# Optimization experiments

Hardware: AMD Instinct MI355X
Metric: run time of the kernel (lower is better)

Reference implementation:

```python
import jax, jax.numpy as jnp
import numpy as np

B, L, HID, H, D = 1, 2048, 3072, 24, 128
MLP = 4 * HID
LH, LW = 32, 56      # latent mask grid -> LH*LW image tokens at the END of the sequence
LIP = 16             # IP-adapter image tokens
IP_SCALE = 0.6


def setup_inputs() -> dict:
    key = jax.random.key(0)
    k = jax.random.split(key, 10)
    # Flux rotary pe layout [1,1,L,D//2,2,2]: pe[...,0]=[cos,-sin], pe[...,1]=[sin,cos]
    pos = jnp.arange(L, dtype=jnp.float32)
    freqs = 1.0 / (10000.0 ** (jnp.arange(0, D, 2, dtype=jnp.float32) / D))
    ang = pos[:, None] * freqs[None, :]            # [L, D//2]
    cos, sin = jnp.cos(ang), jnp.sin(ang)
    pe = jnp.stack([jnp.stack([cos, -sin], -1), jnp.stack([sin, cos], -1)], -2)[None, None]
    return {
        "x": jax.random.normal(k[0], (B, L, HID), jnp.float32),
        "vec": jax.random.normal(k[1], (B, HID), jnp.float32),
        "pe": pe,
        "img_mask": jax.random.uniform(k[2], (B, LH, LW), jnp.float32),
        "image_emb": jax.random.normal(k[3], (B, LIP, HID), jnp.float32),
        "mod_w": jax.random.normal(k[4], (3 * HID, HID), jnp.float32) * 0.02,
        "mod_b": jnp.zeros((3 * HID,), jnp.float32),
        "lin1_w": jax.random.normal(k[5], (3 * HID + MLP, HID), jnp.float32) * 0.02,
        "lin1_b": jnp.zeros((3 * HID + MLP,), jnp.float32),
        "q_scale": jnp.ones((D,), jnp.float32),
        "k_scale": jnp.ones((D,), jnp.float32),
        "lin2_w": jax.random.normal(k[6], (HID, HID + MLP), jnp.float32) * 0.02,
        "lin2_b": jnp.zeros((HID,), jnp.float32),
        "ipk_w": jax.random.normal(k[7], (HID, HID), jnp.float32) * 0.02,
        "ipv_w": jax.random.normal(k[8], (HID, HID), jnp.float32) * 0.02,
    }


def _rms(x, scale, eps):
    # RMSNorm over last dim (QKNorm / norm_added_k)
    return x * jax.lax.rsqrt(jnp.mean(x * x, -1, keepdims=True) + eps) * scale


def _apply_rope(x, pe):
    # x: [B,H,L,D]; pe: [1,1,L,D//2,2,2]
    xr = x.reshape(x.shape[:-1] + (D // 2, 1, 2))
    out = pe[..., 0] * xr[..., 0] + pe[..., 1] * xr[..., 1]  # [B,H,L,D//2,2]
    return out.reshape(x.shape)


def _sdpa(q, k, v):
    # q:[B,H,Lq,D] k,v:[B,H,Lk,D] -> [B,Lq,H*D]
    s = jnp.einsum('bhqd,bhkd->bhqk', q, k) / jnp.sqrt(jnp.float32(D))
    o = jnp.einsum('bhqk,bhkd->bhqd', jax.nn.softmax(s, -1), v)
    return o.transpose(0, 2, 1, 3).reshape(q.shape[0], q.shape[2], H * D)


def reference(x, vec, pe, img_mask, image_emb, mod_w, mod_b, lin1_w, lin1_b,
              q_scale, k_scale, lin2_w, lin2_b, ipk_w, ipv_w):
    # modulation: SiLU(vec) -> Linear -> (shift, scale, gate), each [B,1,HID]
    mod = jax.nn.silu(vec) @ mod_w.T + mod_b
    shift, scale, gate = [m[:, None, :] for m in jnp.split(mod, 3, -1)]
    # pre_norm: LayerNorm, no affine, eps 1e-6 (biased variance, matches torch)
    ln = (x - jnp.mean(x, -1, keepdims=True)) * jax.lax.rsqrt(jnp.var(x, -1, keepdims=True) + 1e-6)
    x_mod = (1.0 + scale) * ln + shift
    # fused qkv + mlp projection
    h = x_mod @ lin1_w.T + lin1_b
    qkv, mlp = h[..., :3 * HID], h[..., 3 * HID:]
    q, k, v = qkv.reshape(B, L, 3, H, D).transpose(2, 0, 3, 1, 4)  # each [B,H,L,D]
    q = _rms(q, q_scale, 1e-6)
    k = _rms(k, k_scale, 1e-6)
    # rp_attention: RoPE then SDPA
    attn = _sdpa(_apply_rope(q, pe), _apply_rope(k, pe), v)       # [B,L,HID]
    # IP-adapter cross-attention: pre-rope q attends to projected image_emb
    ip_k = _rms((image_emb @ ipk_w.T).reshape(B, LIP, H, D).transpose(0, 2, 1, 3), 1.0, 1e-5)
    ip_v = (image_emb @ ipv_w.T).reshape(B, LIP, H, D).transpose(0, 2, 1, 3)
    ip_h = IP_SCALE * _sdpa(q, ip_k, ip_v)                        # [B,L,HID]
    # spatial mask applied to last LH*LW tokens, zeros elsewhere
    full_mask = jnp.concatenate(
        [jnp.zeros((B, L - LH * LW), ip_h.dtype), img_mask.reshape(B, LH * LW)], 1)
    attn = attn + ip_h * full_mask[..., None]
    out = jnp.concatenate([attn, jax.nn.gelu(mlp, approximate=True)], -1) @ lin2_w.T + lin2_b
    return x + gate * out
```

## Files before the change

kernel.cpp:

```cpp
#include <hip/hip_runtime.h>

#define HID 3072
#define LSEQ 2048
#define NH 24
#define HD 128
#define N1 21504
#define K2 15360

typedef unsigned short ushort_t;
typedef __attribute__((ext_vector_type(8))) short bf16x8;
typedef __attribute__((ext_vector_type(4))) float f32x4;

__device__ __forceinline__ unsigned short f2bf(float f) {
    union { float f; unsigned int u; } v; v.f = f;
    unsigned int u = v.u;
    u += 0x7fffu + ((u >> 16) & 1u);
    return (unsigned short)(u >> 16);
}
__device__ __forceinline__ float bf2f(unsigned short s) {
    union { unsigned int u; float f; } v; v.u = ((unsigned int)s) << 16;
    return v.f;
}
__device__ __forceinline__ float gelu_tanh(float x) {
    float u = 0.7978845608028654f * (x + 0.044715f * x * x * x);
    float t = 2.0f / (1.0f + __expf(-2.0f * u)) - 1.0f;
    return 0.5f * x * (1.0f + t);
}
__device__ __forceinline__ void gload_lds16(const ushort_t* g, ushort_t* l) {
    __builtin_amdgcn_global_load_lds((const __attribute__((address_space(1))) void*)g,
                                     (__attribute__((address_space(3))) void*)l, 16, 0, 0);
}

__global__ __launch_bounds__(256) void k_cvt2(const float* __restrict__ s1,
    ushort_t* __restrict__ d1, int n1, const float* __restrict__ s2,
    ushort_t* __restrict__ d2, int n2)
{
    int stride = gridDim.x * 256 * 8;
    int base = (blockIdx.x * 256 + threadIdx.x) * 8;
    for (int i = base; i < n1; i += stride) {
        float4 a = *reinterpret_cast<const float4*>(s1 + i);
        float4 b = *reinterpret_cast<const float4*>(s1 + i + 4);
        uint4 pk;
        pk.x = (unsigned)f2bf(a.x) | ((unsigned)f2bf(a.y) << 16);
        pk.y = (unsigned)f2bf(a.z) | ((unsigned)f2bf(a.w) << 16);
        pk.z = (unsigned)f2bf(b.x) | ((unsigned)f2bf(b.y) << 16);
        pk.w = (unsigned)f2bf(b.z) | ((unsigned)f2bf(b.w) << 16);
        *reinterpret_cast<uint4*>(d1 + i) = pk;
    }
    for (int i = base; i < n2; i += stride) {
        float4 a = *reinterpret_cast<const float4*>(s2 + i);
        float4 b = *reinterpret_cast<const float4*>(s2 + i + 4);
        uint4 pk;
        pk.x = (unsigned)f2bf(a.x) | ((unsigned)f2bf(a.y) << 16);
        pk.y = (unsigned)f2bf(a.z) | ((unsigned)f2bf(a.w) << 16);
        pk.z = (unsigned)f2bf(b.x) | ((unsigned)f2bf(b.y) << 16);
        pk.w = (unsigned)f2bf(b.z) | ((unsigned)f2bf(b.w) << 16);
        *reinterpret_cast<uint4*>(d2 + i) = pk;
    }
}

__global__ __launch_bounds__(256) void k_mod(const float* __restrict__ vec,
    const float* __restrict__ mw, const float* __restrict__ mb, float* __restrict__ mod) {
    __shared__ __align__(16) float sv[HID];
    int tid = threadIdx.x;
    for (int i = tid; i < HID; i += 256) {
        float v = vec[i];
        sv[i] = v / (1.0f + __expf(-v));
    }
    __syncthreads();
    int wave = tid >> 6, lane = tid & 63;
    int n = blockIdx.x * 4 + wave;
    const float* w = mw + (size_t)n * HID;
    float acc = 0.0f;
    for (int k = lane * 4; k < HID; k += 256) {
        float4 wv = *reinterpret_cast<const float4*>(w + k);
        float4 s  = *reinterpret_cast<const float4*>(sv + k);
        acc += wv.x * s.x + wv.y * s.y + wv.z * s.z + wv.w * s.w;
    }
    #pragma unroll
    for (int off = 1; off < 64; off <<= 1) acc += __shfl_xor(acc, off);
    if (lane == 0) mod[n] = acc + mb[n];
}

__global__ __launch_bounds__(256) void k_lnmod(const float* __restrict__ x,
    const float* __restrict__ mod, ushort_t* __restrict__ xmod) {
    int row = blockIdx.x, tid = threadIdx.x;
    const float4* xr = reinterpret_cast<const float4*>(x + (size_t)row * HID);
    float4 v[3];
    float s = 0.f, sq = 0.f;
    #pragma unroll
    for (int i = 0; i < 3; ++i) {
        v[i] = xr[tid + i * 256];
        s  += v[i].x + v[i].y + v[i].z + v[i].w;
        sq += v[i].x * v[i].x + v[i].y * v[i].y + v[i].z * v[i].z + v[i].w * v[i].w;
    }
    #pragma unroll
    for (int off = 1; off < 64; off <<= 1) { s += __shfl_xor(s, off); sq += __shfl_xor(sq, off); }
    __shared__ float rs[4], rq[4];
    int wave = tid >> 6, lane = tid & 63;
    if (lane == 0) { rs[wave] = s; rq[wave] = sq; }
    __syncthreads();
    s  = rs[0] + rs[1] + rs[2] + rs[3];
    sq = rq[0] + rq[1] + rq[2] + rq[3];
    float mean = s * (1.0f / HID);
    float var = sq * (1.0f / HID) - mean * mean;
    float rstd = rsqrtf(var + 1e-6f);
    ushort_t* orow = xmod + (size_t)row * HID;
    #pragma unroll
    for (int i = 0; i < 3; ++i) {
        int c = (tid + i * 256) * 4;
        float4 sc = *reinterpret_cast<const float4*>(mod + HID + c);
        float4 sh = *reinterpret_cast<const float4*>(mod + c);
        float o0 = (1.f + sc.x) * ((v[i].x - mean) * rstd) + sh.x;
        float o1 = (1.f + sc.y) * ((v[i].y - mean) * rstd) + sh.y;
        float o2 = (1.f + sc.z) * ((v[i].z - mean) * rstd) + sh.z;
        float o3 = (1.f + sc.w) * ((v[i].w - mean) * rstd) + sh.w;
        *reinterpret_cast<ushort4*>(orow + c) = make_ushort4(f2bf(o0), f2bf(o1), f2bf(o2), f2bf(o3));
    }
}

#define MFMA_CLUSTER(PH, AF)                                                          \
    do {                                                                              \
        __builtin_amdgcn_s_setprio(1);                                                \
        _Pragma("unroll") for (int i_ = 0; i_ < 2; ++i_)                              \
        _Pragma("unroll") for (int nj_ = 0; nj_ < 4; ++nj_)                           \
        _Pragma("unroll") for (int kh_ = 0; kh_ < 2; ++kh_)                           \
            acc[2 * (PH) + i_][nj_] = __builtin_amdgcn_mfma_f32_16x16x32_bf16(        \
                AF[i_][kh_], bfrag[nj_][kh_], acc[2 * (PH) + i_][nj_], 0, 0, 0);      \
        __builtin_amdgcn_s_setprio(0);                                                \
    } while (0)

__global__ __launch_bounds__(512) void k_gemm8(
    const ushort_t* __restrict__ A, const ushort_t* __restrict__ W,
    const float* __restrict__ bias,
    ushort_t* __restrict__ out_qkv, ushort_t* __restrict__ out_concat)
{
    extern __shared__ __align__(16) char smem_raw[];
    ushort_t* smem = (ushort_t*)smem_raw;
    const int Ks = HID;
    int tid = threadIdx.x;
    int wid = tid >> 6, l = tid & 63;
    int wm = wid >> 2, wn = wid & 3;
    int lr = l & 15, lg = l >> 4;

    int flat = blockIdx.y * 84 + blockIdx.x;
    int nf = (flat & 7) * 84 + (flat >> 3);
    int mt = nf & 7, nt = nf >> 3;
    int m0 = mt * 256, n0 = nt * 256;
    int NT = Ks >> 6;

    int lrow = l >> 3;
    int lc   = (l & 7) ^ lrow;
    int arow_st = wm * 128 + wn * 32 + lrow;
    int bhalf = wn >> 1, ridx = wm * 2 + (wn & 1);
    int brow_st = bhalf * 128 + ridx * 32 + lrow;
    const ushort_t* aSrc = A + (size_t)(m0 + arow_st) * Ks + lc * 8;
    const ushort_t* bSrc = W + (size_t)(n0 + brow_st) * Ks + lc * 8;
    int aDst = (wm * 128 + wn * 32) * 64;
    int bDst = (bhalf * 128 + ridx * 32) * 64;

    auto stageA = [&](int t, int buf, int c) {
        gload_lds16(aSrc + (size_t)c * 8 * Ks + (size_t)t * 64,
                    smem + buf * 16384 + aDst + c * 512);
    };
    auto stageB = [&](int t, int c) {
        gload_lds16(bSrc + (size_t)c * 8 * Ks + (size_t)t * 64,
                    smem + 49152 + (t & 1) * 16384 + bDst + c * 512);
    };
    auto readA = [&](int buf, int row, int ccc) {
        return *reinterpret_cast<const bf16x8*>(smem + buf * 16384 + row * 64 + ((ccc ^ (row & 7)) << 3));
    };
    auto readB = [&](int p, int row, int ccc) {
        return *reinterpret_cast<const bf16x8*>(smem + 49152 + p * 16384 + row * 64 + ((ccc ^ (row & 7)) << 3));
    };

    f32x4 acc[8][4] = {};

    #pragma unroll
    for (int c = 0; c < 4; ++c) stageA(0, 0, c);
    #pragma unroll
    for (int c = 0; c < 4; ++c) stageB(0, c);
    #pragma unroll
    for (int c = 0; c < 4; ++c) stageA(1, 1, c);
    #pragma unroll
    for (int c = 0; c < 4; ++c) stageB(1, c);
    asm volatile("s_waitcnt vmcnt(8)" ::: "memory");
    __builtin_amdgcn_s_barrier();

    int pA = 0, pA2 = 2;
    for (int t = 0; t < NT; ++t) {
        int pB = t & 1;
        bf16x8 bfrag[4][2], af0[2][2], af1[2][2], af2[2][2], af3[2][2];
        #pragma unroll
        for (int nj = 0; nj < 4; ++nj)
            #pragma unroll
            for (int kh = 0; kh < 2; ++kh)
                bfrag[nj][kh] = readB(pB, wn * 64 + nj * 16 + lr, kh * 4 + lg);
        #pragma unroll
        for (int i = 0; i < 2; ++i)
            #pragma unroll
            for (int kh = 0; kh < 2; ++kh)
                af0[i][kh] = readA(pA, wm * 128 + i * 16 + lr, kh * 4 + lg);
        if (t + 2 < NT) {
            stageA(t + 2, pA2, 0); stageA(t + 2, pA2, 1);
            stageA(t + 2, pA2, 2); stageA(t + 2, pA2, 3);
        }
        #pragma unroll
        for (int i = 0; i < 2; ++i)
            #pragma unroll
            for (int kh = 0; kh < 2; ++kh)
                af1[i][kh] = readA(pA, wm * 128 + (2 + i) * 16 + lr, kh * 4 + lg);
        MFMA_CLUSTER(0, af0);
        #pragma unroll
        for (int i = 0; i < 2; ++i)
            #pragma unroll
            for (int kh = 0; kh < 2; ++kh)
                af2[i][kh] = readA(pA, wm * 128 + (4 + i) * 16 + lr, kh * 4 + lg);
        MFMA_CLUSTER(1, af1);
        __builtin_amdgcn_s_barrier();
        if (t + 2 < NT) {
            stageB(t + 2, 0); stageB(t + 2, 1);
            stageB(t + 2, 2); stageB(t + 2, 3);
        }
        #pragma unroll
        for (int i = 0; i < 2; ++i)
            #pragma unroll
            for (int kh = 0; kh < 2; ++kh)
                af3[i][kh] = readA(pA, wm * 128 + (6 + i) * 16 + lr, kh * 4 + lg);
        MFMA_CLUSTER(2, af2);
        MFMA_CLUSTER(3, af3);
        if (t + 2 < NT)      asm volatile("s_waitcnt vmcnt(8)" ::: "memory");
        else if (t + 1 < NT) asm volatile("s_waitcnt vmcnt(0)" ::: "memory");
        __builtin_amdgcn_s_barrier();
        pA  = (pA  + 1 == 3) ? 0 : pA  + 1;
        pA2 = (pA2 + 1 == 3) ? 0 : pA2 + 1;
    }

    #pragma unroll
    for (int nj = 0; nj < 4; ++nj) {
        int col = n0 + wn * 64 + nj * 16 + lr;
        float b = bias[col];
        #pragma unroll
        for (int mi = 0; mi < 8; ++mi) {
            int rbase = m0 + wm * 128 + mi * 16 + lg * 4;
            #pragma unroll
            for (int r = 0; r < 4; ++r) {
                int mrow = rbase + r;
                float val = acc[mi][nj][r] + b;
                if (col < 3 * HID) {
                    out_qkv[(size_t)mrow * (3 * HID) + col] = f2bf(val);
                } else {
                    out_concat[(size_t)mrow * K2 + HID + (col - 3 * HID)] = f2bf(gelu_tanh(val));
                }
            }
        }
    }
}

#define MFMA_CL4(PH, AF)                                                              \
    do {                                                                              \
        __builtin_amdgcn_s_setprio(1);                                                \
        _Pragma("unroll") for (int nj_ = 0; nj_ < 4; ++nj_)                           \
        _Pragma("unroll") for (int kh_ = 0; kh_ < 2; ++kh_)                           \
            acc[(PH)][nj_] = __builtin_amdgcn_mfma_f32_16x16x32_bf16(                 \
                AF[kh_], bfrag[nj_][kh_], acc[(PH)][nj_], 0, 0, 0);                   \
        __builtin_amdgcn_s_setprio(0);                                                \
    } while (0)

__global__ __launch_bounds__(256) void k_gemm4(
    const ushort_t* __restrict__ A, const ushort_t* __restrict__ W,
    int klen, ushort_t* __restrict__ part)
{
    extern __shared__ __align__(16) char smem_raw[];
    ushort_t* smem = (ushort_t*)smem_raw;
    const int Ks = K2;
    int tid = threadIdx.x;
    int wave = tid >> 6, l = tid & 63;
    int wm = wave >> 1, wn = wave & 1;
    int lr = l & 15, lg = l >> 4;

    int flat = blockIdx.y * 24 + blockIdx.x;
    int nf = (flat & 7) * 48 + (flat >> 3);
    int mt = nf & 15, nt = nf >> 4;
    int m0 = mt * 128, n0 = nt * 128;
    int koff = blockIdx.z * klen;
    int NT = klen >> 6;

    int lrow = l >> 3;
    int lc   = (l & 7) ^ lrow;
    const ushort_t* aSrc = A + (size_t)(m0 + wave * 32 + lrow) * Ks + koff + lc * 8;
    const ushort_t* bSrc = W + (size_t)(n0 + wave * 32 + lrow) * Ks + koff + lc * 8;
    int dstBase = wave * 2048;

    auto stageA = [&](int t, int buf) {
        #pragma unroll
        for (int c = 0; c < 4; ++c)
            gload_lds16(aSrc + (size_t)c * 8 * Ks + (size_t)t * 64,
                        smem + buf * 8192 + dstBase + c * 512);
    };
    auto stageB = [&](int t) {
        #pragma unroll
        for (int c = 0; c < 4; ++c)
            gload_lds16(bSrc + (size_t)c * 8 * Ks + (size_t)t * 64,
                        smem + 24576 + (t & 1) * 8192 + dstBase + c * 512);
    };
    auto readA = [&](int buf, int row, int ccc) {
        return *reinterpret_cast<const bf16x8*>(smem + buf * 8192 + row * 64 + ((ccc ^ (row & 7)) << 3));
    };
    auto readB = [&](int p, int row, int ccc) {
        return *reinterpret_cast<const bf16x8*>(smem + 24576 + p * 8192 + row * 64 + ((ccc ^ (row & 7)) << 3));
    };

    f32x4 acc[4][4] = {};

    stageA(0, 0); stageB(0); stageA(1, 1); stageB(1);
    asm volatile("s_waitcnt vmcnt(8)" ::: "memory");
    __builtin_amdgcn_s_barrier();

    int pA = 0, pA2 = 2;
    for (int t = 0; t < NT; ++t) {
        int pB = t & 1;
        bf16x8 bfrag[4][2], af0[2], af1[2], af2[2], af3[2];
        #pragma unroll
        for (int nj = 0; nj < 4; ++nj)
            #pragma unroll
            for (int kh = 0; kh < 2; ++kh)
                bfrag[nj][kh] = readB(pB, wn * 64 + nj * 16 + lr, kh * 4 + lg);
        #pragma unroll
        for (int kh = 0; kh < 2; ++kh)
            af0[kh] = readA(pA, wm * 64 + lr, kh * 4 + lg);
        if (t + 2 < NT) stageA(t + 2, pA2);
        #pragma unroll
        for (int kh = 0; kh < 2; ++kh)
            af1[kh] = readA(pA, wm * 64 + 16 + lr, kh * 4 + lg);
        MFMA_CL4(0, af0);
        #pragma unroll
        for (int kh = 0; kh < 2; ++kh)
            af2[kh] = readA(pA, wm * 64 + 32 + lr, kh * 4 + lg);
        MFMA_CL4(1, af1);
        __builtin_amdgcn_s_barrier();
        if (t + 2 < NT) stageB(t + 2);
        #pragma unroll
        for (int kh = 0; kh < 2; ++kh)
            af3[kh] = readA(pA, wm * 64 + 48 + lr, kh * 4 + lg);
        MFMA_CL4(2, af2);
        MFMA_CL4(3, af3);
        if (t + 2 < NT)      asm volatile("s_waitcnt vmcnt(8)" ::: "memory");
        else if (t + 1 < NT) asm volatile("s_waitcnt vmcnt(0)" ::: "memory");
        __builtin_amdgcn_s_barrier();
        pA  = (pA  + 1 == 3) ? 0 : pA  + 1;
        pA2 = (pA2 + 1 == 3) ? 0 : pA2 + 1;
    }

    #pragma unroll
    for (int nj = 0; nj < 4; ++nj) {
        int col = n0 + wn * 64 + nj * 16 + lr;
        #pragma unroll
        for (int mi = 0; mi < 4; ++mi) {
            int rbase = m0 + wm * 64 + mi * 16 + lg * 4;
            #pragma unroll
            for (int r = 0; r < 4; ++r) {
                int mrow = rbase + r;
                part[(size_t)blockIdx.z * LSEQ * HID + (size_t)mrow * HID + col] = f2bf(acc[mi][nj][r]);
            }
        }
    }
}

__global__ __launch_bounds__(256) void k_red(const ushort_t* __restrict__ part,
    const float* __restrict__ bias, const float* __restrict__ xres,
    const float* __restrict__ mod, float* __restrict__ dout)
{
    size_t base = ((size_t)blockIdx.x * 256 + threadIdx.x) * 8;
    int col = (int)(base % HID);
    float s[8] = {0.f, 0.f, 0.f, 0.f, 0.f, 0.f, 0.f, 0.f};
    #pragma unroll
    for (int z = 0; z < 4; ++z) {
        uint4 pv = *reinterpret_cast<const uint4*>(part + (size_t)z * LSEQ * HID + base);
        unsigned w0 = pv.x, w1 = pv.y, w2 = pv.z, w3 = pv.w;
        s[0] += bf2f((ushort_t)(w0 & 0xffffu)); s[1] += bf2f((ushort_t)(w0 >> 16));
        s[2] += bf2f((ushort_t)(w1 & 0xffffu)); s[3] += bf2f((ushort_t)(w1 >> 16));
        s[4] += bf2f((ushort_t)(w2 & 0xffffu)); s[5] += bf2f((ushort_t)(w2 >> 16));
        s[6] += bf2f((ushort_t)(w3 & 0xffffu)); s[7] += bf2f((ushort_t)(w3 >> 16));
    }
    float4 bb0 = *reinterpret_cast<const float4*>(bias + col);
    float4 bb1 = *reinterpret_cast<const float4*>(bias + col + 4);
    float4 gg0 = *reinterpret_cast<const float4*>(mod + 2 * HID + col);
    float4 gg1 = *reinterpret_cast<const float4*>(mod + 2 * HID + col + 4);
    float4 xx0 = *reinterpret_cast<const float4*>(xres + base);
    float4 xx1 = *reinterpret_cast<const float4*>(xres + base + 4);
    float4 o0, o1;
    o0.x = xx0.x + gg0.x * (s[0] + bb0.x);
    o0.y = xx0.y + gg0.y * (s[1] + bb0.y);
    o0.z = xx0.z + gg0.z * (s[2] + bb0.z);
    o0.w = xx0.w + gg0.w * (s[3] + bb0.w);
    o1.x = xx1.x + gg1.x * (s[4] + bb1.x);
    o1.y = xx1.y + gg1.y * (s[5] + bb1.y);
    o1.z = xx1.z + gg1.z * (s[6] + bb1.z);
    o1.w = xx1.w + gg1.w * (s[7] + bb1.w);
    *reinterpret_cast<float4*>(dout + base) = o0;
    *reinterpret_cast<float4*>(dout + base + 4) = o1;
}

__global__ __launch_bounds__(256) void k_qkv(const ushort_t* __restrict__ qkv,
    const float* __restrict__ pe, const float* __restrict__ q_scale, const float* __restrict__ k_scale,
    ushort_t* __restrict__ q_rope, ushort_t* __restrict__ k_rope,
    ushort_t* __restrict__ q_rms, ushort_t* __restrict__ v_t)
{
    __shared__ ushort_t vtile[64][132];
    int h = blockIdx.y, l0 = blockIdx.x * 64;
    int wave = threadIdx.x >> 6, lane = threadIdx.x & 63;
    int d0 = lane * 2;
    float qs0 = q_scale[d0], qs1 = q_scale[d0 + 1];
    float ks0 = k_scale[d0], ks1 = k_scale[d0 + 1];
    for (int it = 0; it < 16; ++it) {
        int ll = it * 4 + wave;
        int l = l0 + ll;
        const ushort_t* base = qkv + (size_t)l * (3 * HID) + h * HD + d0;
        unsigned qw = *reinterpret_cast<const unsigned*>(base);
        unsigned kw = *reinterpret_cast<const unsigned*>(base + HID);
        unsigned vw = *reinterpret_cast<const unsigned*>(base + 2 * HID);
        float qx = bf2f((ushort_t)(qw & 0xffffu)), qy = bf2f((ushort_t)(qw >> 16));
        float kx = bf2f((ushort_t)(kw & 0xffffu)), ky = bf2f((ushort_t)(kw >> 16));
        float sq = qx * qx + qy * qy;
        float sk = kx * kx + ky * ky;
        #pragma unroll
        for (int off = 1; off < 64; off <<= 1) { sq += __shfl_xor(sq, off); sk += __shfl_xor(sk, off); }
        float rqv = rsqrtf(sq * (1.0f / HD) + 1e-6f);
        float rkv = rsqrtf(sk * (1.0f / HD) + 1e-6f);
        float qnx = qx * rqv * qs0, qny = qy * rqv * qs1;
        float knx = kx * rkv * ks0, kny = ky * rkv * ks1;
        float4 p = *reinterpret_cast<const float4*>(pe + ((size_t)l * 64 + lane) * 4);
        size_t off_hl = ((size_t)h * LSEQ + l) * HD + d0;
        *reinterpret_cast<unsigned*>(q_rms + off_hl) = (unsigned)f2bf(qnx) | ((unsigned)f2bf(qny) << 16);
        float qrx = p.x * qnx + p.y * qny, qry = p.z * qnx + p.w * qny;
        float krx = p.x * knx + p.y * kny, kry = p.z * knx + p.w * kny;
        *reinterpret_cast<unsigned*>(q_rope + off_hl) = (unsigned)f2bf(qrx) | ((unsigned)f2bf(qry) << 16);
        *reinterpret_cast<unsigned*>(k_rope + off_hl) = (unsigned)f2bf(krx) | ((unsigned)f2bf(kry) << 16);
        vtile[ll][d0] = (ushort_t)(vw & 0xffffu);
        vtile[ll][d0 + 1] = (ushort_t)(vw >> 16);
    }
    __syncthreads();
    int d = threadIdx.x >> 1, half = threadIdx.x & 1;
    ushort_t* dst = v_t + ((size_t)h * HD + d) * LSEQ + l0 + half * 32;
    #pragma unroll
    for (int g = 0; g < 4; ++g) {
        unsigned w0, w1, w2, w3;
        int lb = half * 32 + g * 8;
        w0 = (unsigned)vtile[lb + 0][d] | ((unsigned)vtile[lb + 1][d] << 16);
        w1 = (unsigned)vtile[lb + 2][d] | ((unsigned)vtile[lb + 3][d] << 16);
        w2 = (unsigned)vtile[lb + 4][d] | ((unsigned)vtile[lb + 5][d] << 16);
        w3 = (unsigned)vtile[lb + 6][d] | ((unsigned)vtile[lb + 7][d] << 16);
        reinterpret_cast<uint4*>(dst)[g] = make_uint4(w0, w1, w2, w3);
    }
}

__global__ __launch_bounds__(256) void k_ipgemv(const float* __restrict__ emb,
    const float* __restrict__ wk, const float* __restrict__ wv,
    float* __restrict__ ipk, float* __restrict__ ipv)
{
    int task = blockIdx.x * 4 + (threadIdx.x >> 6);
    int lane = threadIdx.x & 63;
    int which = task / HID;
    int n = task % HID;
    const float* w = (which ? wv : wk) + (size_t)n * HID;
    float acc[16];
    #pragma unroll
    for (int t = 0; t < 16; ++t) acc[t] = 0.f;
    for (int k = lane; k < HID; k += 64) {
        float wval = w[k];
        #pragma unroll
        for (int t = 0; t < 16; ++t) acc[t] += emb[t * HID + k] * wval;
    }
    #pragma unroll
    for (int off = 1; off < 64; off <<= 1) {
        #pragma unroll
        for (int t = 0; t < 16; ++t) acc[t] += __shfl_xor(acc[t], off);
    }
    if (lane == 0) {
        int hh = n >> 7, d = n & 127;
        float* dstp = which ? ipv : ipk;
        #pragma unroll
        for (int t = 0; t < 16; ++t) dstp[((size_t)hh * 16 + t) * HD + d] = acc[t];
    }
}

__global__ __launch_bounds__(256) void k_ipkrms(float* __restrict__ ipk) {
    int row = blockIdx.x * 4 + (threadIdx.x >> 6);
    int lane = threadIdx.x & 63;
    float2 v = *reinterpret_cast<const float2*>(ipk + (size_t)row * HD + lane * 2);
    float sq = v.x * v.x + v.y * v.y;
    #pragma unroll
    for (int off = 1; off < 64; off <<= 1) sq += __shfl_xor(sq, off);
    float r = rsqrtf(sq * (1.0f / HD) + 1e-5f);
    float2 o; o.x = v.x * r; o.y = v.y * r;
    *reinterpret_cast<float2*>(ipk + (size_t)row * HD + lane * 2) = o;
}

__global__ __launch_bounds__(256) void k_attn(const ushort_t* __restrict__ q_rope,
    const ushort_t* __restrict__ k_rope, const ushort_t* __restrict__ v_t,
    ushort_t* __restrict__ concat)
{
    __shared__ __align__(16) ushort_t Ks[64 * 128];
    __shared__ __align__(16) ushort_t Vs[128 * 64];
    __shared__ __align__(16) ushort_t Ps[4 * 16 * 72];
    const float SC = 0.08838834764831845f;
    int h = blockIdx.y, q0 = blockIdx.x * 64;
    int tid = threadIdx.x, wave = tid >> 6, lane = tid & 63;
    int lr = lane & 15, lg = lane >> 4;
    const ushort_t* Kb = k_rope + (size_t)h * LSEQ * HD;
    const ushort_t* Vb = v_t + (size_t)h * HD * LSEQ;
    bf16x8 qf[4];
    #pragma unroll
    for (int ks = 0; ks < 4; ++ks) {
        int row = q0 + wave * 16 + lr;
        qf[ks] = *reinterpret_cast<const bf16x8*>(q_rope + ((size_t)h * LSEQ + row) * HD + ks * 32 + lg * 8);
    }
    f32x4 o[8] = {};
    float mrun[4], lrun[4];
    #pragma unroll
    for (int r = 0; r < 4; ++r) { mrun[r] = -1e30f; lrun[r] = 0.f; }

    for (int kt = 0; kt < LSEQ; kt += 64) {
        #pragma unroll
        for (int ii = 0; ii < 4; ++ii) {
            int c = tid + ii * 256;
            int krow = c >> 4, kc = c & 15;
            uint4 va = *reinterpret_cast<const uint4*>(Kb + (size_t)(kt + krow) * HD + kc * 8);
            *reinterpret_cast<uint4*>(reinterpret_cast<char*>(Ks) + krow * 256 + ((kc ^ (krow & 15)) << 4)) = va;
            int dr = c >> 3, vc = c & 7;
            uint4 vb = *reinterpret_cast<const uint4*>(Vb + (size_t)dr * LSEQ + kt + vc * 8);
            *reinterpret_cast<uint4*>(reinterpret_cast<char*>(Vs) + dr * 128 + ((vc ^ (dr & 7)) << 4)) = vb;
        }
        __syncthreads();
        f32x4 s[4] = {};
        __builtin_amdgcn_s_setprio(1);
        #pragma unroll
        for (int ks = 0; ks < 4; ++ks) {
            bf16x8 kf[4];
            #pragma unroll
            for (int j = 0; j < 4; ++j) {
                int krow = j * 16 + lr;
                int cc = ks * 4 + lg;
                kf[j] = *reinterpret_cast<const bf16x8*>(reinterpret_cast<char*>(Ks) + krow * 256 + ((cc ^ (krow & 15)) << 4));
            }
            #pragma unroll
            for (int j = 0; j < 4; ++j)
                s[j] = __builtin_amdgcn_mfma_f32_16x16x32_bf16(qf[ks], kf[j], s[j], 0, 0, 0);
        }
        __builtin_amdgcn_s_setprio(0);
        float alpha[4];
        #pragma unroll
        for (int r = 0; r < 4; ++r) {
            float v0 = s[0][r] * SC, v1 = s[1][r] * SC;
            float v2 = s[2][r] * SC, v3 = s[3][r] * SC;
            float mx = fmaxf(fmaxf(v0, v1), fmaxf(v2, v3));
            #pragma unroll
            for (int off = 1; off < 16; off <<= 1) mx = fmaxf(mx, __shfl_xor(mx, off));
            float mnew = fmaxf(mrun[r], mx);
            float al = __expf(mrun[r] - mnew);
            float p0 = __expf(v0 - mnew), p1 = __expf(v1 - mnew);
            float p2 = __expf(v2 - mnew), p3 = __expf(v3 - mnew);
            float rs2 = p0 + p1 + p2 + p3;
            #pragma unroll
            for (int off = 1; off < 16; off <<= 1) rs2 += __shfl_xor(rs2, off);
            lrun[r] = lrun[r] * al + rs2;
            mrun[r] = mnew;
            alpha[r] = al;
            s[0][r] = p0; s[1][r] = p1; s[2][r] = p2; s[3][r] = p3;
        }
        #pragma unroll
        for (int j8 = 0; j8 < 8; ++j8)
            #pragma unroll
            for (int r = 0; r < 4; ++r) o[j8][r] *= alpha[r];
        #pragma unroll
        for (int j = 0; j < 4; ++j)
            #pragma unroll
            for (int r = 0; r < 4; ++r) {
                int ql = lg * 4 + r;
                Ps[wave * 1152 + ql * 72 + j * 16 + lr] = f2bf(s[j][r]);
            }
        __syncthreads();
        bf16x8 pa[2];
        #pragma unroll
        for (int ks2 = 0; ks2 < 2; ++ks2)
            pa[ks2] = *reinterpret_cast<const bf16x8*>(Ps + wave * 1152 + lr * 72 + ks2 * 32 + lg * 8);
        __builtin_amdgcn_s_setprio(1);
        #pragma unroll
        for (int j8 = 0; j8 < 8; ++j8) {
            int d = j8 * 16 + lr;
            #pragma unroll
            for (int ks2 = 0; ks2 < 2; ++ks2) {
                int cc = ks2 * 4 + lg;
                bf16x8 vf = *reinterpret_cast<const bf16x8*>(reinterpret_cast<char*>(Vs) + d * 128 + ((cc ^ (d & 7)) << 4));
                o[j8] = __builtin_amdgcn_mfma_f32_16x16x32_bf16(pa[ks2], vf, o[j8], 0, 0, 0);
            }
        }
        __builtin_amdgcn_s_setprio(0);
        __syncthreads();
    }
    #pragma unroll
    for (int r = 0; r < 4; ++r) {
        float inv = 1.0f / lrun[r];
        int mrow = q0 + wave * 16 + lg * 4 + r;
        ushort_t* crow = concat + (size_t)mrow * K2 + h * HD;
        #pragma unroll
        for (int j8 = 0; j8 < 8; ++j8)
            crow[j8 * 16 + lr] = f2bf(o[j8][r] * inv);
    }
}

__global__ __launch_bounds__(256) void k_ipattn(const ushort_t* __restrict__ q_rms,
    const float* __restrict__ ipk, const float* __restrict__ ipv,
    const float* __restrict__ img_mask, ushort_t* __restrict__ concat)
{
    int task = blockIdx.x * 4 + (threadIdx.x >> 6);
    int lane = threadIdx.x & 63;
    int h = task / 1792;
    int l = 256 + task % 1792;
    int d0 = lane * 2;
    float mask = img_mask[l - 256];
    unsigned cw = *reinterpret_cast<const unsigned*>(concat + (size_t)l * K2 + h * HD + d0);
    float ax = bf2f((ushort_t)(cw & 0xffffu)), ay = bf2f((ushort_t)(cw >> 16));
    unsigned qv = *reinterpret_cast<const unsigned*>(q_rms + ((size_t)h * LSEQ + l) * HD + d0);
    float qx = bf2f((ushort_t)(qv & 0xffffu)), qy = bf2f((ushort_t)(qv >> 16));
    float s[16];
    const float* kb = ipk + (size_t)h * 16 * HD + d0;
    #pragma unroll
    for (int j = 0; j < 16; ++j) {
        float2 kk = *reinterpret_cast<const float2*>(kb + j * HD);
        float part = qx * kk.x + qy * kk.y;
        #pragma unroll
        for (int off = 1; off < 64; off <<= 1) part += __shfl_xor(part, off);
        s[j] = part * 0.08838834764831845f;
    }
    float mx = s[0];
    #pragma unroll
    for (int j = 1; j < 16; ++j) mx = fmaxf(mx, s[j]);
    float sum = 0.f;
    #pragma unroll
    for (int j = 0; j < 16; ++j) { s[j] = __expf(s[j] - mx); sum += s[j]; }
    float ox = 0.f, oy = 0.f;
    const float* vb = ipv + (size_t)h * 16 * HD + d0;
    #pragma unroll
    for (int j = 0; j < 16; ++j) {
        float2 vv = *reinterpret_cast<const float2*>(vb + j * HD);
        ox += s[j] * vv.x; oy += s[j] * vv.y;
    }
    float f = 0.6f * mask / sum;
    ax += f * ox; ay += f * oy;
    *reinterpret_cast<unsigned*>(concat + (size_t)l * K2 + h * HD + d0) =
        (unsigned)f2bf(ax) | ((unsigned)f2bf(ay) << 16);
}

extern "C" void kernel_launch(void* const* d_in, const int* in_sizes, int n_in,
                              void* d_out, int out_size, void* d_ws, size_t ws_size,
                              hipStream_t stream)
{
    (void)in_sizes; (void)n_in; (void)out_size; (void)ws_size;
    const float* x         = (const float*)d_in[0];
    const float* vec       = (const float*)d_in[1];
    const float* pe        = (const float*)d_in[2];
    const float* img_mask  = (const float*)d_in[3];
    const float* image_emb = (const float*)d_in[4];
    const float* mod_w     = (const float*)d_in[5];
    const float* mod_b     = (const float*)d_in[6];
    const float* lin1_w    = (const float*)d_in[7];
    const float* lin1_b    = (const float*)d_in[8];
    const float* q_scale   = (const float*)d_in[9];
    const float* k_scale   = (const float*)d_in[10];
    const float* lin2_w    = (const float*)d_in[11];
    const float* lin2_b    = (const float*)d_in[12];
    const float* ipk_w     = (const float*)d_in[13];
    const float* ipv_w     = (const float*)d_in[14];
    float* dout = (float*)d_out;

    char* wp = (char*)d_ws;
    auto alloc = [&](size_t bytes) { char* p = wp; wp += (bytes + 255) & ~(size_t)255; return p; };
    float*    mod     = (float*)   alloc((size_t)9216 * 4);
    ushort_t* concat  = (ushort_t*)alloc((size_t)LSEQ * K2 * 2);
    ushort_t* lin2_bf = (ushort_t*)alloc((size_t)HID * K2 * 2);
    float*    ipk     = (float*)   alloc((size_t)NH * 16 * HD * 4);
    float*    ipv     = (float*)   alloc((size_t)NH * 16 * HD * 4);
    char* ubase = wp;
    ushort_t* lin1_bf = (ushort_t*)alloc((size_t)N1 * HID * 2);
    ushort_t* xmod    = (ushort_t*)alloc((size_t)LSEQ * HID * 2);
    ushort_t* qkv     = (ushort_t*)alloc((size_t)LSEQ * 3 * HID * 2);
    ushort_t* q_rope  = (ushort_t*)alloc((size_t)NH * LSEQ * HD * 2);
    ushort_t* k_rope  = (ushort_t*)alloc((size_t)NH * LSEQ * HD * 2);
    ushort_t* q_rms   = (ushort_t*)alloc((size_t)NH * LSEQ * HD * 2);
    ushort_t* v_t     = (ushort_t*)alloc((size_t)NH * HD * LSEQ * 2);
    ushort_t* partial = (ushort_t*)ubase;

    hipFuncSetAttribute((const void*)k_gemm8, hipFuncAttributeMaxDynamicSharedMemorySize, 163840);
    hipFuncSetAttribute((const void*)k_gemm4, hipFuncAttributeMaxDynamicSharedMemorySize, 81920);

    k_cvt2  <<<dim3(4096), dim3(256), 0, stream>>>(lin1_w, lin1_bf, N1 * HID,
                                                   lin2_w, lin2_bf, HID * K2);
    k_mod   <<<dim3(9216 / 4), dim3(256), 0, stream>>>(vec, mod_w, mod_b, mod);
    k_lnmod <<<dim3(LSEQ), dim3(256), 0, stream>>>(x, mod, xmod);
    k_gemm8 <<<dim3(84, 8), dim3(512), 163840, stream>>>(xmod, lin1_bf, lin1_b, qkv, concat);
    k_qkv   <<<dim3(32, NH), dim3(256), 0, stream>>>(qkv, pe, q_scale, k_scale,
                                                     q_rope, k_rope, q_rms, v_t);
    k_ipgemv<<<dim3(2 * HID / 4), dim3(256), 0, stream>>>(image_emb, ipk_w, ipv_w, ipk, ipv);
    k_ipkrms<<<dim3(NH * 16 / 4), dim3(256), 0, stream>>>(ipk);
    k_attn  <<<dim3(32, NH), dim3(256), 0, stream>>>(q_rope, k_rope, v_t, concat);
    k_ipattn<<<dim3(NH * 1792 / 4), dim3(256), 0, stream>>>(q_rms, ipk, ipv, img_mask, concat);
    k_gemm4 <<<dim3(24, 16, 4), dim3(256), 81920, stream>>>(concat, lin2_bf, 3840, partial);
    k_red   <<<dim3(LSEQ * HID / 2048), dim3(256), 0, stream>>>(partial, lin2_b, x, mod, dout);
}
```

Measured before the change: 946.8 us.

## Use 4 waves per block with 128x128 warp tiles in lin1 GEMM

The lin1 GEMM kernel drops from 8 waves of 512 threads, each computing a 128x64 sub-tile, to 4 waves of 256 threads, each computing a 128x128 sub-tile of the same 256x256 block tile. Each wave now loads 8 B fragments and streams A fragments row by row, so more MFMAs run per LDS read and fewer waves contend for LDS. The cost is a 64-entry accumulator array per thread, which raises register pressure, and less latency hiding from fewer waves per CU. Global-to-LDS staging is rebalanced so each wave issues 8 loads per operand, and the wait counts are adjusted to match.

```diff
diff --git a/kernel.cpp b/kernel.cpp
--- a/kernel.cpp
+++ b/kernel.cpp
@@ -119,18 +119,17 @@
     }
 }
 
-#define MFMA_CLUSTER(PH, AF)                                                          \
+#define MFMA_M(MI, AF)                                                                \
     do {                                                                              \
         __builtin_amdgcn_s_setprio(1);                                                \
-        _Pragma("unroll") for (int i_ = 0; i_ < 2; ++i_)                              \
-        _Pragma("unroll") for (int nj_ = 0; nj_ < 4; ++nj_)                           \
+        _Pragma("unroll") for (int nj_ = 0; nj_ < 8; ++nj_)                           \
         _Pragma("unroll") for (int kh_ = 0; kh_ < 2; ++kh_)                           \
-            acc[2 * (PH) + i_][nj_] = __builtin_amdgcn_mfma_f32_16x16x32_bf16(        \
-                AF[i_][kh_], bfrag[nj_][kh_], acc[2 * (PH) + i_][nj_], 0, 0, 0);      \
+            acc[(MI)][nj_] = __builtin_amdgcn_mfma_f32_16x16x32_bf16(                 \
+                AF[kh_], bfrag[nj_][kh_], acc[(MI)][nj_], 0, 0, 0);                   \
         __builtin_amdgcn_s_setprio(0);                                                \
     } while (0)
 
-__global__ __launch_bounds__(512) void k_gemm8(
+__global__ __launch_bounds__(256) void k_gemm8(
     const ushort_t* __restrict__ A, const ushort_t* __restrict__ W,
     const float* __restrict__ bias,
     ushort_t* __restrict__ out_qkv, ushort_t* __restrict__ out_concat)
@@ -139,8 +138,8 @@
     ushort_t* smem = (ushort_t*)smem_raw;
     const int Ks = HID;
     int tid = threadIdx.x;
-    int wid = tid >> 6, l = tid & 63;
-    int wm = wid >> 2, wn = wid & 3;
+    int w = tid >> 6, l = tid & 63;
+    int wm = w >> 1, wn = w & 1;
     int lr = l & 15, lg = l >> 4;
 
     int flat = blockIdx.y * 84 + blockIdx.x;
@@ -151,21 +150,21 @@
 
     int lrow = l >> 3;
     int lc   = (l & 7) ^ lrow;
-    int arow_st = wm * 128 + wn * 32 + lrow;
-    int bhalf = wn >> 1, ridx = wm * 2 + (wn & 1);
-    int brow_st = bhalf * 128 + ridx * 32 + lrow;
-    const ushort_t* aSrc = A + (size_t)(m0 + arow_st) * Ks + lc * 8;
-    const ushort_t* bSrc = W + (size_t)(n0 + brow_st) * Ks + lc * 8;
-    int aDst = (wm * 128 + wn * 32) * 64;
-    int bDst = (bhalf * 128 + ridx * 32) * 64;
-
-    auto stageA = [&](int t, int buf, int c) {
-        gload_lds16(aSrc + (size_t)c * 8 * Ks + (size_t)t * 64,
-                    smem + buf * 16384 + aDst + c * 512);
+    const ushort_t* aSrc = A + (size_t)(m0 + w * 64 + lrow) * Ks + lc * 8;
+    const ushort_t* bSrc = W + (size_t)(n0 + w * 64 + lrow) * Ks + lc * 8;
+    int dstBase = w * 4096;
+
+    auto stageA = [&](int t, int buf) {
+        #pragma unroll
+        for (int c = 0; c < 8; ++c)
+            gload_lds16(aSrc + (size_t)c * 8 * Ks + (size_t)t * 64,
+                        smem + buf * 16384 + dstBase + c * 512);
     };
-    auto stageB = [&](int t, int c) {
-        gload_lds16(bSrc + (size_t)c * 8 * Ks + (size_t)t * 64,
-                    smem + 49152 + (t & 1) * 16384 + bDst + c * 512);
+    auto stageB = [&](int t) {
+        #pragma unroll
+        for (int c = 0; c < 8; ++c)
+            gload_lds16(bSrc + (size_t)c * 8 * Ks + (size_t)t * 64,
+                        smem + 49152 + (t & 1) * 16384 + dstBase + c * 512);
     };
     auto readA = [&](int buf, int row, int ccc) {
         return *reinterpret_cast<const bf16x8*>(smem + buf * 16384 + row * 64 + ((ccc ^ (row & 7)) << 3));
@@ -174,62 +173,57 @@
         return *reinterpret_cast<const bf16x8*>(smem + 49152 + p * 16384 + row * 64 + ((ccc ^ (row & 7)) << 3));
     };
 
-    f32x4 acc[8][4] = {};
-
-    #pragma unroll
-    for (int c = 0; c < 4; ++c) stageA(0, 0, c);
-    #pragma unroll
-    for (int c = 0; c < 4; ++c) stageB(0, c);
-    #pragma unroll
-    for (int c = 0; c < 4; ++c) stageA(1, 1, c);
-    #pragma unroll
-    for (int c = 0; c < 4; ++c) stageB(1, c);
-    asm volatile("s_waitcnt vmcnt(8)" ::: "memory");
+    f32x4 acc[8][8] = {};
+
+    stageA(0, 0); stageB(0); stageA(1, 1); stageB(1);
+    asm volatile("s_waitcnt vmcnt(16)" ::: "memory");
     __builtin_amdgcn_s_barrier();
 
     int pA = 0, pA2 = 2;
     for (int t = 0; t < NT; ++t) {
         int pB = t & 1;
-        bf16x8 bfrag[4][2], af0[2][2], af1[2][2], af2[2][2], af3[2][2];
-        #pragma unroll
-        for (int nj = 0; nj < 4; ++nj)
+        bf16x8 bfrag[8][2], afA[2], afB[2];
+        #pragma unroll
+        for (int nj = 0; nj < 8; ++nj)
             #pragma unroll
             for (int kh = 0; kh < 2; ++kh)
-                bfrag[nj][kh] = readB(pB, wn * 64 + nj * 16 + lr, kh * 4 + lg);
-        #pragma unroll
-        for (int i = 0; i < 2; ++i)
-            #pragma unroll
-            for (int kh = 0; kh < 2; ++kh)
-                af0[i][kh] = readA(pA, wm * 128 + i * 16 + lr, kh * 4 + lg);
-        if (t + 2 < NT) {
-            stageA(t + 2, pA2, 0); stageA(t + 2, pA2, 1);
-            stageA(t + 2, pA2, 2); stageA(t + 2, pA2, 3);
-        }
-        #pragma unroll
-        for (int i = 0; i < 2; ++i)
-            #pragma unroll
-            for (int kh = 0; kh < 2; ++kh)
-                af1[i][kh] = readA(pA, wm * 128 + (2 + i) * 16 + lr, kh * 4 + lg);
-        MFMA_CLUSTER(0, af0);
-        #pragma unroll
-        for (int i = 0; i < 2; ++i)
-            #pragma unroll
-            for (int kh = 0; kh < 2; ++kh)
-                af2[i][kh] = readA(pA, wm * 128 + (4 + i) * 16 + lr, kh * 4 + lg);
-        MFMA_CLUSTER(1, af1);
+                bfrag[nj][kh] = readB(pB, wn * 128 + nj * 16 + lr, kh * 4 + lg);
+        #pragma unroll
+        for (int kh = 0; kh < 2; ++kh)
+            afA[kh] = readA(pA, wm * 128 + lr, kh * 4 + lg);
+        if (t + 2 < NT) stageA(t + 2, pA2);
+        #pragma unroll
+        for (int kh = 0; kh < 2; ++kh)
+            afB[kh] = readA(pA, wm * 128 + 16 + lr, kh * 4 + lg);
+        MFMA_M(0, afA);
+        #pragma unroll
+        for (int kh = 0; kh < 2; ++kh)
+            afA[kh] = readA(pA, wm * 128 + 32 + lr, kh * 4 + lg);
+        MFMA_M(1, afB);
+        #pragma unroll
+        for (int kh = 0; kh < 2; ++kh)
+            afB[kh] = readA(pA, wm * 128 + 48 + lr, kh * 4 + lg);
+        MFMA_M(2, afA);
         __builtin_amdgcn_s_barrier();
-        if (t + 2 < NT) {
-            stageB(t + 2, 0); stageB(t + 2, 1);
-            stageB(t + 2, 2); stageB(t + 2, 3);
-        }
-        #pragma unroll
-        for (int i = 0; i < 2; ++i)
-            #pragma unroll
-            for (int kh = 0; kh < 2; ++kh)
-                af3[i][kh] = readA(pA, wm * 128 + (6 + i) * 16 + lr, kh * 4 + lg);
-        MFMA_CLUSTER(2, af2);
-        MFMA_CLUSTER(3, af3);
-        if (t + 2 < NT)      asm volatile("s_waitcnt vmcnt(8)" ::: "memory");
+        if (t + 2 < NT) stageB(t + 2);
+        #pragma unroll
+        for (int kh = 0; kh < 2; ++kh)
+            afA[kh] = readA(pA, wm * 128 + 64 + lr, kh * 4 + lg);
+        MFMA_M(3, afB);
+        #pragma unroll
+        for (int kh = 0; kh < 2; ++kh)
+            afB[kh] = readA(pA, wm * 128 + 80 + lr, kh * 4 + lg);
+        MFMA_M(4, afA);
+        #pragma unroll
+        for (int kh = 0; kh < 2; ++kh)
+            afA[kh] = readA(pA, wm * 128 + 96 + lr, kh * 4 + lg);
+        MFMA_M(5, afB);
+        #pragma unroll
+        for (int kh = 0; kh < 2; ++kh)
+            afB[kh] = readA(pA, wm * 128 + 112 + lr, kh * 4 + lg);
+        MFMA_M(6, afA);
+        MFMA_M(7, afB);
+        if (t + 2 < NT)      asm volatile("s_waitcnt vmcnt(16)" ::: "memory");
         else if (t + 1 < NT) asm volatile("s_waitcnt vmcnt(0)" ::: "memory");
         __builtin_amdgcn_s_barrier();
         pA  = (pA  + 1 == 3) ? 0 : pA  + 1;
@@ -237,8 +231,8 @@
     }
 
     #pragma unroll
-    for (int nj = 0; nj < 4; ++nj) {
-        int col = n0 + wn * 64 + nj * 16 + lr;
+    for (int nj = 0; nj < 8; ++nj) {
+        int col = n0 + wn * 128 + nj * 16 + lr;
         float b = bias[col];
         #pragma unroll
         for (int mi = 0; mi < 8; ++mi) {
@@ -699,7 +693,7 @@
                                                    lin2_w, lin2_bf, HID * K2);
     k_mod   <<<dim3(9216 / 4), dim3(256), 0, stream>>>(vec, mod_w, mod_b, mod);
     k_lnmod <<<dim3(LSEQ), dim3(256), 0, stream>>>(x, mod, xmod);
-    k_gemm8 <<<dim3(84, 8), dim3(512), 163840, stream>>>(xmod, lin1_bf, lin1_b, qkv, concat);
+    k_gemm8 <<<dim3(84, 8), dim3(256), 163840, stream>>>(xmod, lin1_bf, lin1_b, qkv, concat);
     k_qkv   <<<dim3(32, NH), dim3(256), 0, stream>>>(qkv, pe, q_scale, k_scale,
                                                      q_rope, k_rope, q_rms, v_t);
     k_ipgemv<<<dim3(2 * HID / 4), dim3(256), 0, stream>>>(image_emb, ipk_w, ipv_w, ipk, ipv);
```

New measurement: 995.2 us. 1.05x slower.
